# Kernel tuning notes

Measured on AMD Instinct MI355X. Metric: run time of the kernel, lower is better.

Reference implementation:

```python
import jax, jax.numpy as jnp
import numpy as np

N = 8192        # num nodes, > sparse_attention_threshold=5000 -> sparse attention path
IN = 128        # in_channels
OUT = 128       # out_channels
HEADS = 2       # attention_heads
DEG = 32        # avg degree used to build theta sparsity


def _xavier(key, shape):
    a = np.sqrt(6.0 / (shape[0] + shape[1])).astype(np.float32)
    return jax.random.uniform(key, shape, jnp.float32, -a, a)


def setup_inputs() -> dict:
    rng = np.random.default_rng(0)
    rows = np.repeat(np.arange(N), DEG)
    cols = rng.integers(0, N, size=N * DEG)
    theta_np = np.zeros((N, N), dtype=np.float32)
    theta_np[rows, cols] = 1.0
    # matches torch: rows, cols = np.where(theta > 1e-5)
    r, c = np.nonzero(theta_np > 1e-5)
    edge_index = jnp.asarray(np.stack([r, c]).astype(np.int32))  # [2, E]
    key = jax.random.key(0)
    ks = jax.random.split(key, 4)
    x = jax.random.normal(ks[0], (N, IN), jnp.float32)
    weight = _xavier(ks[1], (IN, OUT * HEADS))
    bias = jnp.zeros((OUT * HEADS,), jnp.float32)
    att_weight1 = _xavier(ks[2], (2 * OUT, OUT // 2))
    att_weight2 = _xavier(ks[3], (OUT // 2, 1))
    return {"x": x, "theta": jnp.asarray(theta_np), "weight": weight,
            "bias": bias, "att_weight1": att_weight1,
            "att_weight2": att_weight2, "edge_index": edge_index}


def _forward(x, weight, bias, att_weight1, att_weight2, edge_index):
    # x @ W + b, reshape to [N, heads, out]
    h = (x @ weight + bias).reshape(N, HEADS, OUT)
    src, dst = edge_index[0], edge_index[1]
    # cat([h_src, h_dst]) @ W1 == h_src @ W1[:OUT] + h_dst @ W1[OUT:]
    # project at node level first (cheaper), then gather per edge
    p_src = jnp.einsum('nhd,df->nhf', h, att_weight1[:OUT])
    p_dst = jnp.einsum('nhd,df->nhf', h, att_weight1[OUT:])
    s = jax.nn.leaky_relu(p_src[src] + p_dst[dst])               # [E, H, OUT//2]
    scores = jnp.einsum('ehf,fo->eho', s, att_weight2)[..., 0]    # [E, H]
    # torch does F.softmax(att_scores, dim=0): GLOBAL softmax over all edges per head
    att = jax.nn.softmax(scores, axis=0)                          # [E, H]
    # sparse COO mm: out[src] += att * h[dst]
    msgs = att[:, :, None] * h[dst]                               # [E, H, OUT]
    agg = jnp.zeros((N, HEADS, OUT), h.dtype).at[src].add(msgs)
    return agg.mean(axis=1)                                       # mean over heads -> [N, OUT]


def reference(x, theta, weight, bias, att_weight1, att_weight2, edge_index):
    # theta only determines the edge list (computed on CPU/numpy in the torch
    # code); edge_index is precomputed consistently in setup_inputs.
    del theta
    return _forward(x, weight, bias, att_weight1, att_weight2, edge_index)
```

## Files before the change

### kernel.cpp

```cpp
#include <hip/hip_runtime.h>
#include <hip/hip_bf16.h>

#define NN 8192
#define INC 128
#define HC 256
#define NPB 8

__global__ __launch_bounds__(256) void k_h_p(
    const float* __restrict__ x, const float* __restrict__ W,
    const float* __restrict__ bias, const float* __restrict__ att1,
    float* __restrict__ h, float* __restrict__ ps, float* __restrict__ pd,
    float* __restrict__ sums) {
  int t = threadIdx.x;
  int n0 = blockIdx.x * NPB;
  if (blockIdx.x == 0 && t < 2) sums[t] = 0.f;
  __shared__ float xs[NPB][INC];
  __shared__ float hs[NPB][HC];
  ((float4*)&xs[0][0])[t] = ((const float4*)(x + (size_t)n0 * INC))[t];
  __syncthreads();
  float acc[NPB];
  float b = bias[t];
  #pragma unroll
  for (int n = 0; n < NPB; ++n) acc[n] = b;
  #pragma unroll 4
  for (int d = 0; d < INC; ++d) {
    float w = W[d * HC + t];
    #pragma unroll
    for (int n = 0; n < NPB; ++n) acc[n] += xs[n][d] * w;
  }
  #pragma unroll
  for (int n = 0; n < NPB; ++n) {
    h[((size_t)(n0 + n)) * HC + t] = acc[n];
    hs[n][t] = acc[n];
  }
  __syncthreads();
  int f = t & 63, sel = t >> 6;
  int hh = sel & 1, isdst = sel >> 1;
  const float* a1 = att1 + (isdst ? 128 * 64 : 0) + f;
  float p[NPB];
  #pragma unroll
  for (int n = 0; n < NPB; ++n) p[n] = 0.f;
  #pragma unroll 4
  for (int d = 0; d < 128; ++d) {
    float w = a1[d * 64];
    #pragma unroll
    for (int n = 0; n < NPB; ++n) p[n] += hs[n][hh * 128 + d] * w;
  }
  float* dp = isdst ? pd : ps;
  #pragma unroll
  for (int n = 0; n < NPB; ++n)
    dp[((size_t)(n0 + n)) * 128 + hh * 64 + f] = p[n];
}

#define SCORE_BLOCKS 1024
__global__ __launch_bounds__(256) void k_score(
    const float* __restrict__ ps, const float* __restrict__ pd,
    const int* __restrict__ ei, const float* __restrict__ att2,
    float* __restrict__ exps, float* __restrict__ sums,
    int* __restrict__ offs, int E) {
  __shared__ float w2[64];
  __shared__ float ssum[2];
  int t = threadIdx.x;
  if (t < 64) w2[t] = att2[t];
  if (t < 2) ssum[t] = 0.f;
  __syncthreads();
  int g = t >> 4, sub = t & 15;
  int total = E * 2;
  float runsum = 0.f;
  for (int pair = blockIdx.x * 16 + g; pair < total; pair += SCORE_BLOCKS * 16) {
    int hh = pair & 1;
    int e = pair >> 1;
    int s = ei[e], dt = ei[E + e];
    float4 av = *(const float4*)&ps[((size_t)s * 2 + hh) * 64 + sub * 4];
    float4 bv = *(const float4*)&pd[((size_t)dt * 2 + hh) * 64 + sub * 4];
    float vx = av.x + bv.x; vx = vx > 0.f ? vx : 0.01f * vx;
    float vy = av.y + bv.y; vy = vy > 0.f ? vy : 0.01f * vy;
    float vz = av.z + bv.z; vz = vz > 0.f ? vz : 0.01f * vz;
    float vw = av.w + bv.w; vw = vw > 0.f ? vw : 0.01f * vw;
    float sc = vx * w2[sub * 4] + vy * w2[sub * 4 + 1] + vz * w2[sub * 4 + 2] + vw * w2[sub * 4 + 3];
    #pragma unroll
    for (int off = 8; off; off >>= 1) sc += __shfl_down(sc, off, 16);
    if (sub == 0) {
      float ev = expf(sc);
      exps[pair] = ev;
      runsum += ev;
      if (hh == 0) {
        if (e == 0) offs[0] = 0;
        else if (ei[e] != ei[e - 1]) offs[ei[e]] = e;
        if (e == E - 1) offs[NN] = E;
      }
    }
  }
  runsum += __shfl_xor(runsum, 32);
  int lane = t & 63;
  if (lane == 0 || lane == 16) atomicAdd(&ssum[(t >> 4) & 1], runsum);
  __syncthreads();
  if (t < 2) atomicAdd(&sums[t], ssum[t]);
}

__global__ __launch_bounds__(256) void k_agg(
    const float* __restrict__ h, const float* __restrict__ exps,
    const float* __restrict__ sums, const int* __restrict__ ei,
    const int* __restrict__ offs, float* __restrict__ out, int E) {
  int n = blockIdx.x, t = threadIdx.x;
  int lo = offs[n], hi = offs[n + 1];
  int hh = t >> 7;
  float inv = 1.0f / sums[hh];
  float acc = 0.f;
  for (int e = lo; e < hi; ++e) {
    int dst = ei[E + e];
    float w = exps[e * 2 + hh];
    acc += w * h[(size_t)dst * HC + t];
  }
  acc *= inv;
  __shared__ float l[HC];
  l[t] = acc;
  __syncthreads();
  if (t < 128)
    out[(size_t)n * 128 + t] = 0.5f * (l[t] + l[128 + t]);
}

extern "C" void kernel_launch(void* const* d_in, const int* in_sizes, int n_in,
                              void* d_out, int out_size, void* d_ws, size_t ws_size,
                              hipStream_t stream) {
  const float* x    = (const float*)d_in[0];
  const float* W    = (const float*)d_in[2];
  const float* bias = (const float*)d_in[3];
  const float* att1 = (const float*)d_in[4];
  const float* att2 = (const float*)d_in[5];
  const int* ei = (const int*)d_in[6];
  int E = in_sizes[6] / 2;
  float* out = (float*)d_out;

  float* ws = (float*)d_ws;
  float* h      = ws;
  float* ps     = h  + (size_t)NN * HC;
  float* pd     = ps + (size_t)NN * 128;
  float* exps   = pd + (size_t)NN * 128;
  float* sums   = exps + (size_t)E * 2;
  int*   offs   = (int*)(sums + 2);

  k_h_p<<<NN / NPB, 256, 0, stream>>>(x, W, bias, att1, h, ps, pd, sums);
  k_score<<<SCORE_BLOCKS, 256, 0, stream>>>(ps, pd, ei, att2, exps, sums, offs, E);
  k_agg<<<NN, 256, 0, stream>>>(h, exps, sums, ei, offs, out, E);
}
```

Baseline: 433.8 us.

## Fuse three kernels into one cooperative persistent kernel with grid syncs

Merges the projection, score/exp, and aggregation kernels into one cooperative kernel of 512 persistent blocks that uses grid.sync between phases. If the cooperative launch fails it falls back to the separate kernels. It also switches expf to __expf and unrolls the aggregation gather by four to keep more loads in flight. The aim is to remove launch gaps between stages, at the cost of fewer blocks in the aggregation phase, grid-barrier overhead, and a slightly less accurate exponential.

After: 623.8 us. +43.8%, slower.

```diff
diff --git a/kernel.cpp b/kernel.cpp
--- a/kernel.cpp
+++ b/kernel.cpp
@@ -1,22 +1,23 @@
 #include <hip/hip_runtime.h>
-#include <hip/hip_bf16.h>
+#include <hip/hip_cooperative_groups.h>
+
+namespace cg = cooperative_groups;
 
 #define NN 8192
 #define INC 128
 #define HC 256
 #define NPB 8
-
-__global__ __launch_bounds__(256) void k_h_p(
-    const float* __restrict__ x, const float* __restrict__ W,
+#define NGRP (NN / NPB)
+#define NB 512
+#define SCORE_BLOCKS 1024
+
+__device__ __forceinline__ void phaseA_group(
+    int grp, int t, const float* __restrict__ x, const float* __restrict__ W,
     const float* __restrict__ bias, const float* __restrict__ att1,
     float* __restrict__ h, float* __restrict__ ps, float* __restrict__ pd,
-    float* __restrict__ sums) {
-  int t = threadIdx.x;
-  int n0 = blockIdx.x * NPB;
-  if (blockIdx.x == 0 && t < 2) sums[t] = 0.f;
-  __shared__ float xs[NPB][INC];
-  __shared__ float hs[NPB][HC];
-  ((float4*)&xs[0][0])[t] = ((const float4*)(x + (size_t)n0 * INC))[t];
+    float* xs, float* hs) {
+  int n0 = grp * NPB;
+  ((float4*)xs)[t] = ((const float4*)(x + (size_t)n0 * INC))[t];
   __syncthreads();
   float acc[NPB];
   float b = bias[t];
@@ -26,12 +27,12 @@
   for (int d = 0; d < INC; ++d) {
     float w = W[d * HC + t];
     #pragma unroll
-    for (int n = 0; n < NPB; ++n) acc[n] += xs[n][d] * w;
+    for (int n = 0; n < NPB; ++n) acc[n] += xs[n * INC + d] * w;
   }
   #pragma unroll
   for (int n = 0; n < NPB; ++n) {
     h[((size_t)(n0 + n)) * HC + t] = acc[n];
-    hs[n][t] = acc[n];
+    hs[n * HC + t] = acc[n];
   }
   __syncthreads();
   int f = t & 63, sel = t >> 6;
@@ -44,7 +45,7 @@
   for (int d = 0; d < 128; ++d) {
     float w = a1[d * 64];
     #pragma unroll
-    for (int n = 0; n < NPB; ++n) p[n] += hs[n][hh * 128 + d] * w;
+    for (int n = 0; n < NPB; ++n) p[n] += hs[n * HC + hh * 128 + d] * w;
   }
   float* dp = isdst ? pd : ps;
   #pragma unroll
@@ -52,22 +53,20 @@
     dp[((size_t)(n0 + n)) * 128 + hh * 64 + f] = p[n];
 }
 
-#define SCORE_BLOCKS 1024
-__global__ __launch_bounds__(256) void k_score(
-    const float* __restrict__ ps, const float* __restrict__ pd,
-    const int* __restrict__ ei, const float* __restrict__ att2,
-    float* __restrict__ exps, float* __restrict__ sums,
-    int* __restrict__ offs, int E) {
-  __shared__ float w2[64];
-  __shared__ float ssum[2];
-  int t = threadIdx.x;
+__device__ __forceinline__ void phaseB(
+    int bid, int nblocks, int t, const float* __restrict__ ps,
+    const float* __restrict__ pd, const int* __restrict__ ei,
+    const float* __restrict__ att2, float* __restrict__ exps,
+    float* __restrict__ sums, int* __restrict__ offs, int E, float* smem) {
+  float* w2 = smem;
+  float* ssum = smem + 64;
   if (t < 64) w2[t] = att2[t];
   if (t < 2) ssum[t] = 0.f;
   __syncthreads();
   int g = t >> 4, sub = t & 15;
   int total = E * 2;
   float runsum = 0.f;
-  for (int pair = blockIdx.x * 16 + g; pair < total; pair += SCORE_BLOCKS * 16) {
+  for (int pair = bid * 16 + g; pair < total; pair += nblocks * 16) {
     int hh = pair & 1;
     int e = pair >> 1;
     int s = ei[e], dt = ei[E + e];
@@ -81,7 +80,7 @@
     #pragma unroll
     for (int off = 8; off; off >>= 1) sc += __shfl_down(sc, off, 16);
     if (sub == 0) {
-      float ev = expf(sc);
+      float ev = __expf(sc);
       exps[pair] = ev;
       runsum += ev;
       if (hh == 0) {
@@ -98,26 +97,84 @@
   if (t < 2) atomicAdd(&sums[t], ssum[t]);
 }
 
-__global__ __launch_bounds__(256) void k_agg(
+__device__ __forceinline__ void phaseC_node(
+    int n, int t, int hh, float inv, const float* __restrict__ h,
+    const float* __restrict__ exps, const int* __restrict__ ei,
+    const int* __restrict__ offs, float* __restrict__ out, int E, float* l) {
+  int lo = offs[n], hi = offs[n + 1];
+  float acc = 0.f;
+  int e = lo;
+  for (; e + 4 <= hi; e += 4) {
+    int d0 = ei[E + e], d1 = ei[E + e + 1], d2 = ei[E + e + 2], d3 = ei[E + e + 3];
+    float w0 = exps[2 * e + hh],       w1 = exps[2 * (e + 1) + hh];
+    float w2v = exps[2 * (e + 2) + hh], w3 = exps[2 * (e + 3) + hh];
+    float h0 = h[(size_t)d0 * HC + t], h1 = h[(size_t)d1 * HC + t];
+    float h2 = h[(size_t)d2 * HC + t], h3 = h[(size_t)d3 * HC + t];
+    acc += w0 * h0 + w1 * h1 + w2v * h2 + w3 * h3;
+  }
+  for (; e < hi; ++e)
+    acc += exps[2 * e + hh] * h[(size_t)ei[E + e] * HC + t];
+  acc *= inv;
+  __syncthreads();
+  l[t] = acc;
+  __syncthreads();
+  if (t < 128)
+    out[(size_t)n * 128 + t] = 0.5f * (l[t] + l[128 + t]);
+}
+
+__global__ __launch_bounds__(256, 2) void k_fused(
+    const float* __restrict__ x, const float* __restrict__ W,
+    const float* __restrict__ bias, const float* __restrict__ att1,
+    const float* __restrict__ att2, const int* __restrict__ ei,
+    float* __restrict__ h, float* __restrict__ ps, float* __restrict__ pd,
+    float* __restrict__ exps, float* __restrict__ sums, int* __restrict__ offs,
+    float* __restrict__ out, int E) {
+  cg::grid_group grid = cg::this_grid();
+  __shared__ float smem[NPB * INC + NPB * HC];
+  int t = threadIdx.x, bid = blockIdx.x;
+  if (bid == 0 && t < 2) sums[t] = 0.f;
+  for (int grp = bid; grp < NGRP; grp += NB)
+    phaseA_group(grp, t, x, W, bias, att1, h, ps, pd, smem, smem + NPB * INC);
+  grid.sync();
+  phaseB(bid, NB, t, ps, pd, ei, att2, exps, sums, offs, E, smem);
+  grid.sync();
+  {
+    int hh = t >> 7;
+    float inv = 1.0f / sums[hh];
+    for (int n = bid; n < NN; n += NB)
+      phaseC_node(n, t, hh, inv, h, exps, ei, offs, out, E, smem);
+  }
+}
+
+__global__ __launch_bounds__(256) void k_h_p_sep(
+    const float* __restrict__ x, const float* __restrict__ W,
+    const float* __restrict__ bias, const float* __restrict__ att1,
+    float* __restrict__ h, float* __restrict__ ps, float* __restrict__ pd,
+    float* __restrict__ sums) {
+  __shared__ float smem[NPB * INC + NPB * HC];
+  if (blockIdx.x == 0 && threadIdx.x < 2) sums[threadIdx.x] = 0.f;
+  phaseA_group(blockIdx.x, threadIdx.x, x, W, bias, att1, h, ps, pd,
+               smem, smem + NPB * INC);
+}
+
+__global__ __launch_bounds__(256) void k_score_sep(
+    const float* __restrict__ ps, const float* __restrict__ pd,
+    const int* __restrict__ ei, const float* __restrict__ att2,
+    float* __restrict__ exps, float* __restrict__ sums,
+    int* __restrict__ offs, int E) {
+  __shared__ float smem[66];
+  phaseB(blockIdx.x, SCORE_BLOCKS, threadIdx.x, ps, pd, ei, att2, exps, sums,
+         offs, E, smem);
+}
+
+__global__ __launch_bounds__(256) void k_agg_sep(
     const float* __restrict__ h, const float* __restrict__ exps,
     const float* __restrict__ sums, const int* __restrict__ ei,
     const int* __restrict__ offs, float* __restrict__ out, int E) {
-  int n = blockIdx.x, t = threadIdx.x;
-  int lo = offs[n], hi = offs[n + 1];
-  int hh = t >> 7;
+  __shared__ float l[HC];
+  int t = threadIdx.x, hh = t >> 7;
   float inv = 1.0f / sums[hh];
-  float acc = 0.f;
-  for (int e = lo; e < hi; ++e) {
-    int dst = ei[E + e];
-    float w = exps[e * 2 + hh];
-    acc += w * h[(size_t)dst * HC + t];
-  }
-  acc *= inv;
-  __shared__ float l[HC];
-  l[t] = acc;
-  __syncthreads();
-  if (t < 128)
-    out[(size_t)n * 128 + t] = 0.5f * (l[t] + l[128 + t]);
+  phaseC_node(blockIdx.x, t, hh, inv, h, exps, ei, offs, out, E, l);
 }
 
 extern "C" void kernel_launch(void* const* d_in, const int* in_sizes, int n_in,
@@ -140,7 +197,15 @@
   float* sums   = exps + (size_t)E * 2;
   int*   offs   = (int*)(sums + 2);
 
-  k_h_p<<<NN / NPB, 256, 0, stream>>>(x, W, bias, att1, h, ps, pd, sums);
-  k_score<<<SCORE_BLOCKS, 256, 0, stream>>>(ps, pd, ei, att2, exps, sums, offs, E);
-  k_agg<<<NN, 256, 0, stream>>>(h, exps, sums, ei, offs, out, E);
-}
+  void* args[] = { (void*)&x, (void*)&W, (void*)&bias, (void*)&att1,
+                   (void*)&att2, (void*)&ei, (void*)&h, (void*)&ps,
+                   (void*)&pd, (void*)&exps, (void*)&sums, (void*)&offs,
+                   (void*)&out, (void*)&E };
+  hipError_t err = hipLaunchCooperativeKernel((const void*)k_fused, dim3(NB),
+                                              dim3(256), args, 0, stream);
+  if (err != hipSuccess) {
+    k_h_p_sep<<<NGRP, 256, 0, stream>>>(x, W, bias, att1, h, ps, pd, sums);
+    k_score_sep<<<SCORE_BLOCKS, 256, 0, stream>>>(ps, pd, ei, att2, exps, sums, offs, E);
+    k_agg_sep<<<NN, 256, 0, stream>>>(h, exps, sums, ei, offs, out, E);
+  }
+}
```
